# Performance work log

Hardware: AMD Instinct MI355X
Metric: run time of the kernel (lower is better)

The kernel has to match this reference:

```python
import jax, jax.numpy as jnp
import numpy as np

B, V, N, IN_F, HEADS, OUT_F = 4, 4, 1000, 64, 4, 32
D = HEADS * OUT_F  # 128, concat=True
E = 64000
NEG_SLOPE = 0.2


def setup_inputs() -> dict:
    key = jax.random.key(0)
    ks = jax.random.split(key, 8)
    x = jax.random.normal(ks[0], (B, V, N, IN_F), jnp.float32)
    edge_index = jax.random.randint(ks[1], (2, E), 0, B * N, dtype=jnp.int64)
    W = jax.random.normal(ks[2], (HEADS * OUT_F, IN_F), jnp.float32) / np.sqrt(IN_F)
    att = jax.random.normal(ks[3], (1, HEADS, 2 * OUT_F), jnp.float32) * 0.1
    in_proj_w = jax.random.normal(ks[4], (3 * D, D), jnp.float32) / np.sqrt(D)
    in_proj_b = jnp.zeros((3 * D,), jnp.float32)
    out_proj_w = jax.random.normal(ks[5], (D, D), jnp.float32) / np.sqrt(D)
    out_proj_b = jnp.zeros((D,), jnp.float32)
    bias = jnp.zeros((D,), jnp.float32)
    return dict(x=x, W=W, att=att, in_proj_w=in_proj_w, in_proj_b=in_proj_b,
                out_proj_w=out_proj_w, out_proj_b=out_proj_b, bias=bias,
                edge_index=edge_index)


def reference(x, W, att, in_proj_w, in_proj_b, out_proj_w, out_proj_b, bias, edge_index):
    Bx, Vx, Nx, _ = x.shape
    Ntot = Bx * Nx
    # intra-view GAT: shared W across views
    h = jnp.einsum('bvni,oi->bvno', x, W).reshape(Bx, Vx, Nx, HEADS, OUT_F)
    # block-diagonal placement: h_full[b*V+v, b*N:(b+1)*N] = h[b,v]
    ib = jnp.arange(Bx)
    hf = jnp.zeros((Bx, Vx, Bx, Nx, HEADS, OUT_F), x.dtype).at[ib, :, ib].set(h)
    h_full = hf.reshape(Bx * Vx, Ntot, HEADS, OUT_F)
    # add self loops
    loops = jnp.arange(Ntot, dtype=edge_index.dtype)
    src = jnp.concatenate([edge_index[0], loops])
    dst = jnp.concatenate([edge_index[1], loops])
    # attention scores (faithful to source: flatten h_full over (B*V, Ntot) and
    # index with raw node ids, i.e. gathers from block 0 only)
    h_flat = h_full.reshape(Bx * Vx * Ntot, HEADS, OUT_F)
    h_cat = jnp.concatenate([h_flat[src], h_flat[dst]], axis=-1)  # [Etot, H, 2*OUT]
    att_in = jax.nn.leaky_relu(h_cat, NEG_SLOPE)
    scores = jnp.sum(att * att_in, axis=-1)  # [Etot, HEADS]
    # per-destination segment softmax
    seg_max = jax.ops.segment_max(scores, dst, num_segments=Ntot)
    seg_max = jax.lax.stop_gradient(jnp.where(jnp.isfinite(seg_max), seg_max, 0.0))
    ex = jnp.exp(scores - seg_max[dst])
    denom = jax.ops.segment_sum(ex, dst, num_segments=Ntot)
    alpha = ex / (denom[dst] + 1e-16)  # [Etot, HEADS]
    # scatter-add aggregation, broadcast over B*V rows
    msgs = h_full[:, src] * alpha[None, :, :, None]  # [B*V, Etot, H, OUT]
    out_full = jnp.zeros_like(h_full).at[:, dst].add(msgs)
    # extract each graph's own node block
    out = out_full.reshape(Bx, Vx, Bx, Nx, HEADS, OUT_F)[ib, :, ib]  # [B,V,N,H,OUT]
    h_gat = out.reshape(Bx, Vx, Nx, HEADS * OUT_F)  # concat heads
    # inter-view mixing: MHA over the V axis per node
    seq = h_gat.transpose(0, 2, 1, 3).reshape(Bx * Nx, Vx, D)
    q, k, v = jnp.split(seq @ in_proj_w.T + in_proj_b, 3, axis=-1)
    hd = D // HEADS
    sp = lambda t: t.reshape(Bx * Nx, Vx, HEADS, hd).transpose(0, 2, 1, 3)
    q, k, v = sp(q), sp(k), sp(v)
    aw = jax.nn.softmax(jnp.einsum('bhqd,bhkd->bhqk', q, k) / jnp.sqrt(jnp.asarray(hd, x.dtype)), axis=-1)
    ao = jnp.einsum('bhqk,bhkd->bhqd', aw, v).transpose(0, 2, 1, 3).reshape(Bx * Nx, Vx, D)
    mixed = ao @ out_proj_w.T + out_proj_b
    h_mixed = mixed.reshape(Bx, Nx, Vx, D).transpose(0, 2, 1, 3)  # [B,V,N,D]
    return h_mixed + bias
```

## Files before the change

### kernel.cpp

```cpp
#include <hip/hip_runtime.h>

#define NN 1000
#define HEADS_ 4
#define DM 128
#define EE 64000
#define NTOT 4000
#define ETOT 68000
#define CAP 48
#define EB 34

template <int KK, int SCORE>
__device__ void gemm64(int mi, int ni,
                       const float* __restrict__ A, const float* __restrict__ Wt,
                       const float* __restrict__ b1,
                       float* __restrict__ C, int N,
                       const float* __restrict__ att,
                       float* __restrict__ ssrc, float* __restrict__ sdst) {
  __shared__ float As[64 * 64];
  __shared__ float Bs[64 * 64];
  int tid = threadIdx.x;
  int m0 = mi * 64, n0 = ni * 64;
  int tx = tid & 15, ty = tid >> 4;
  const float4* A4 = (const float4*)A;
  const float4* W4 = (const float4*)Wt;
  float acc[4][4] = {};

  for (int c = 0; c < KK / 64; ++c) {
    __syncthreads();
    {
      int q = tid & 15, r0 = tid >> 4;
#pragma unroll
      for (int p = 0; p < 4; ++p) {
        int r = r0 + p * 16;
        float4 v = A4[(size_t)(m0 + r) * (KK / 4) + c * 16 + q];
        *(float4*)&As[r * 64 + ((q ^ ((r >> 2) & 15)) << 2)] = v;
      }
#pragma unroll
      for (int p = 0; p < 4; ++p) {
        int r = r0 + p * 16;
        float4 v = W4[(size_t)(n0 + r) * (KK / 4) + c * 16 + q];
        *(float4*)&Bs[r * 64 + ((q ^ ((r >> 2) & 15)) << 2)] = v;
      }
    }
    __syncthreads();
#pragma unroll 4
    for (int q = 0; q < 16; ++q) {
      float4 a[4], b[4];
      int sa = (q ^ ty) << 2;
      int sb = (q ^ tx) << 2;
#pragma unroll
      for (int i = 0; i < 4; ++i)
        a[i] = *(const float4*)&As[(ty * 4 + i) * 64 + sa];
#pragma unroll
      for (int j = 0; j < 4; ++j)
        b[j] = *(const float4*)&Bs[(tx * 4 + j) * 64 + sb];
#pragma unroll
      for (int i = 0; i < 4; ++i)
#pragma unroll
        for (int j = 0; j < 4; ++j)
          acc[i][j] += a[i].x * b[j].x + a[i].y * b[j].y
                     + a[i].z * b[j].z + a[i].w * b[j].w;
    }
  }

  int nc = n0 + tx * 4;
  float4 bd = make_float4(0.f, 0.f, 0.f, 0.f);
  if (b1) bd = *(const float4*)&b1[nc];
#pragma unroll
  for (int i = 0; i < 4; ++i) {
    int m = m0 + ty * 4 + i;
    *(float4*)&C[(size_t)m * N + nc] =
        make_float4(acc[i][0] + bd.x, acc[i][1] + bd.y,
                    acc[i][2] + bd.z, acc[i][3] + bd.w);
  }

  if (SCORE && m0 < NN) {
    int hsel = tx >> 3;
    int h = ni * 2 + hsel;
    int kb = (tx & 7) * 4;
    float a0[4], a1[4];
#pragma unroll
    for (int j = 0; j < 4; ++j) {
      a0[j] = att[h * 64 + kb + j];
      a1[j] = att[h * 64 + 32 + kb + j];
    }
#pragma unroll
    for (int i = 0; i < 4; ++i) {
      int m = m0 + ty * 4 + i;
      float p0 = 0.f, p1 = 0.f;
#pragma unroll
      for (int j = 0; j < 4; ++j) {
        float g = acc[i][j];
        float lr = g > 0.f ? g : 0.2f * g;
        p0 += a0[j] * lr;
        p1 += a1[j] * lr;
      }
      p0 += __shfl_xor(p0, 1, 16); p1 += __shfl_xor(p1, 1, 16);
      p0 += __shfl_xor(p0, 2, 16); p1 += __shfl_xor(p1, 2, 16);
      p0 += __shfl_xor(p0, 4, 16); p1 += __shfl_xor(p1, 4, 16);
      if ((tx & 7) == 0 && m < NN) {
        ssrc[m * HEADS_ + h] = p0;
        sdst[m * HEADS_ + h] = p1;
      }
    }
  }
}

__global__ __launch_bounds__(256) void k1_kernel(const float* __restrict__ x,
                                                 const float* __restrict__ W,
                                                 const float* __restrict__ att,
                                                 float* __restrict__ hbuf,
                                                 float* __restrict__ ssrc,
                                                 float* __restrict__ sdst,
                                                 const int* __restrict__ ei,
                                                 int* __restrict__ cnt,
                                                 int* __restrict__ elist) {
  int bid = blockIdx.x;
  if (bid < 500) {
    gemm64<64, 1>(bid >> 1, bid & 1, x, W, nullptr, hbuf, 128, att, ssrc, sdst);
  } else {
    for (int e = (bid - 500) * 256 + threadIdx.x; e < ETOT; e += EB * 256) {
      int s, d;
      if (e < EE) { s = ei[e]; d = ei[EE + e]; }
      else { s = d = e - EE; }
      int pos = atomicAdd(&cnt[d], 1);
      if (pos < CAP) elist[d * CAP + pos] = s;
    }
  }
}

__global__ __launch_bounds__(256) void gather_kernel(const int* __restrict__ cnt,
                                                     const int* __restrict__ elist,
                                                     const float* __restrict__ ssrc,
                                                     const float* __restrict__ sdst,
                                                     const float* __restrict__ hbuf,
                                                     float* __restrict__ hgat) {
  __shared__ int   srcs[2][CAP];
  __shared__ float exs[2][CAP][HEADS_];
  int li = threadIdx.x >> 7;
  int t = threadIdx.x & 127;
  int d = blockIdx.x * 2 + li;
  int b = d / NN;
  int v = t >> 5, q = t & 31, h = q >> 3;
  int m = cnt[d]; if (m > CAP) m = CAP;
  for (int base = 0; base < m; base += 32) {
    int i = base + (t >> 2);
    if (i < m) {
      int s = elist[d * CAP + i];
      if ((t & 3) == 0) srcs[li][i] = s;
      float sc = ssrc[s * HEADS_ + (t & 3)] + sdst[d * HEADS_ + (t & 3)];
      exs[li][i][t & 3] = __expf(sc);
    }
  }
  __syncthreads();
  float den = 1e-16f;
  float4 acc = make_float4(0.f, 0.f, 0.f, 0.f);
  const float* hbase = hbuf + ((size_t)(b * 4 + v) * NN) * DM + q * 4;
  int i = 0;
  for (; i + 4 <= m; i += 4) {
    float ex[4]; unsigned sl[4]; float4 hv[4];
#pragma unroll
    for (int u = 0; u < 4; ++u) {
      ex[u] = exs[li][i + u][h];
      sl[u] = (unsigned)(srcs[li][i + u] - b * NN);
      unsigned sls = sl[u] < NN ? sl[u] : 0u;
      hv[u] = *(const float4*)(hbase + (size_t)sls * DM);
    }
#pragma unroll
    for (int u = 0; u < 4; ++u) {
      den += ex[u];
      float w = sl[u] < NN ? ex[u] : 0.f;
      acc.x += w * hv[u].x; acc.y += w * hv[u].y;
      acc.z += w * hv[u].z; acc.w += w * hv[u].w;
    }
  }
  for (; i < m; ++i) {
    float ex = exs[li][i][h];
    den += ex;
    unsigned sl = (unsigned)(srcs[li][i] - b * NN);
    if (sl < NN) {
      float4 hv = *(const float4*)(hbase + (size_t)sl * DM);
      acc.x += ex * hv.x; acc.y += ex * hv.y;
      acc.z += ex * hv.z; acc.w += ex * hv.w;
    }
  }
  float r = 1.f / den;
  acc.x *= r; acc.y *= r; acc.z *= r; acc.w *= r;
  *(float4*)&hgat[((size_t)(d * 4 + v)) * DM + q * 4] = acc;
}

__global__ __launch_bounds__(256) void qkv_kernel(const float* __restrict__ hgat,
                                                  const float* __restrict__ inw,
                                                  const float* __restrict__ inb,
                                                  float* __restrict__ qkv) {
  gemm64<128, 0>(blockIdx.x, blockIdx.y, hgat, inw, inb, qkv, 384,
                 nullptr, nullptr, nullptr);
}

__global__ __launch_bounds__(256) void attnout_kernel(const float* __restrict__ qkv,
                                                      const float* __restrict__ outw,
                                                      const float* __restrict__ outb,
                                                      const float* __restrict__ bias,
                                                      float* __restrict__ out) {
  __shared__ float smem[20480];
  float* outwS = smem;
  float* aoS   = smem + 16384;

  int tid = threadIdx.x;
  int blk = blockIdx.x;
  int cg = tid & 31, rg = tid >> 5;
  int node0 = blk * 8;

  const float4* Q4 = (const float4*)qkv;
  float4 qf[4], kf[4], vf[4];
#pragma unroll
  for (int vq = 0; vq < 4; ++vq) {
    size_t row = (size_t)((node0 + rg) * 4 + vq) * 96;
    qf[vq] = Q4[row + cg];
    kf[vq] = Q4[row + 32 + cg];
    vf[vq] = Q4[row + 64 + cg];
  }

  const float4* O4 = (const float4*)outw;
#pragma unroll
  for (int tt = 0; tt < 16; ++tt) {
    int g = tt * 256 + tid;
    int kg = g & 7, kc = (g >> 3) & 3, col = g >> 5;
    float4 vv = O4[g];
    *(float4*)&outwS[kc * 4096 + col * 32 + ((kg ^ ((col >> 2) & 7)) << 2)] = vv;
  }

  float S[4][4];
#pragma unroll
  for (int vq = 0; vq < 4; ++vq)
#pragma unroll
    for (int vk = 0; vk < 4; ++vk)
      S[vq][vk] = qf[vq].x * kf[vk].x + qf[vq].y * kf[vk].y
                + qf[vq].z * kf[vk].z + qf[vq].w * kf[vk].w;
#pragma unroll
  for (int vq = 0; vq < 4; ++vq)
#pragma unroll
    for (int vk = 0; vk < 4; ++vk) {
      float s = S[vq][vk];
      s += __shfl_xor(s, 1);
      s += __shfl_xor(s, 2);
      s += __shfl_xor(s, 4);
      S[vq][vk] = s * 0.17677669529663687f;
    }
#pragma unroll
  for (int vq = 0; vq < 4; ++vq) {
    float mx = fmaxf(fmaxf(S[vq][0], S[vq][1]), fmaxf(S[vq][2], S[vq][3]));
    float e0 = __expf(S[vq][0] - mx), e1 = __expf(S[vq][1] - mx);
    float e2 = __expf(S[vq][2] - mx), e3 = __expf(S[vq][3] - mx);
    float inv = 1.f / (e0 + e1 + e2 + e3);
    S[vq][0] = e0 * inv; S[vq][1] = e1 * inv; S[vq][2] = e2 * inv; S[vq][3] = e3 * inv;
  }

  {
    int kc = cg >> 3, d4 = cg & 7;
#pragma unroll
    for (int vq = 0; vq < 4; ++vq) {
      float4 o = make_float4(0.f, 0.f, 0.f, 0.f);
#pragma unroll
      for (int vk = 0; vk < 4; ++vk) {
        float w = S[vq][vk];
        o.x += w * vf[vk].x; o.y += w * vf[vk].y;
        o.z += w * vf[vk].z; o.w += w * vf[vk].w;
      }
      int r = rg * 4 + vq;
      *(float4*)&aoS[kc * 1024 + r * 32 + ((d4 ^ rg) << 2)] = o;
    }
  }
  __syncthreads();

  int rg2 = tid & 7, og = tid >> 3;
  float oc[4][4] = {};
#pragma unroll 2
  for (int kc2 = 0; kc2 < 4; ++kc2) {
#pragma unroll
    for (int q = 0; q < 8; ++q) {
      float4 a[4], bq[4];
      int ga = (q ^ rg2) << 2;
      int gb = (q ^ (og & 7)) << 2;
#pragma unroll
      for (int i = 0; i < 4; ++i)
        a[i] = *(const float4*)&aoS[kc2 * 1024 + (rg2 * 4 + i) * 32 + ga];
#pragma unroll
      for (int j = 0; j < 4; ++j)
        bq[j] = *(const float4*)&outwS[kc2 * 4096 + (og * 4 + j) * 32 + gb];
#pragma unroll
      for (int i = 0; i < 4; ++i)
#pragma unroll
        for (int j = 0; j < 4; ++j)
          oc[i][j] += a[i].x * bq[j].x + a[i].y * bq[j].y
                    + a[i].z * bq[j].z + a[i].w * bq[j].w;
    }
  }

  {
    int nc = og * 4;
    float4 ob = make_float4(outb[nc] + bias[nc], outb[nc + 1] + bias[nc + 1],
                            outb[nc + 2] + bias[nc + 2], outb[nc + 3] + bias[nc + 3]);
#pragma unroll
    for (int i = 0; i < 4; ++i) {
      int node = node0 + rg2, vv = i;
      int bg = node / NN, n = node - bg * NN;
      int om = (bg * 4 + vv) * NN + n;
      *(float4*)&out[(size_t)om * DM + nc] =
          make_float4(oc[i][0] + ob.x, oc[i][1] + ob.y,
                      oc[i][2] + ob.z, oc[i][3] + ob.w);
    }
  }
}

extern "C" void kernel_launch(void* const* d_in, const int* in_sizes, int n_in,
                              void* d_out, int out_size, void* d_ws, size_t ws_size,
                              hipStream_t stream) {
  const float* x    = (const float*)d_in[0];
  const float* W    = (const float*)d_in[1];
  const float* att  = (const float*)d_in[2];
  const float* inw  = (const float*)d_in[3];
  const float* inb  = (const float*)d_in[4];
  const float* outw = (const float*)d_in[5];
  const float* outb = (const float*)d_in[6];
  const float* bias = (const float*)d_in[7];
  const int*   ei   = (const int*)d_in[8];
  float* out = (float*)d_out;

  float* ws = (float*)d_ws;
  float* hbuf  = ws;
  float* hgat  = ws + 2100000;
  float* qkv   = ws + 4200000;
  float* ssrc  = ws + 12500000;
  float* sdst  = ssrc + 16000;
  int*   cnt   = (int*)(sdst + 16000);
  int*   elist = cnt + 4000;

  hipMemsetAsync(ssrc, 0, 36000 * sizeof(float), stream);

  k1_kernel<<<500 + EB, 256, 0, stream>>>(x, W, att, hbuf, ssrc, sdst, ei, cnt, elist);
  gather_kernel<<<NTOT / 2, 256, 0, stream>>>(cnt, elist, ssrc, sdst, hbuf, hgat);
  qkv_kernel<<<dim3(250, 6), 256, 0, stream>>>(hgat, inw, inb, qkv);
  attnout_kernel<<<500, 256, 0, stream>>>(qkv, outw, outb, bias, out);
}
```

Baseline: 148.5 us.

## Fuse GAT gather, QKV projection and view attention into one kernel

Merges the gather/softmax aggregation, the QKV GEMM and the inter-view attention plus output projection into a single kernel per pair of destination nodes. Intermediates stay in shared memory instead of making round trips through global hgat/qkv buffers, and two kernel launches are removed. In exchange, each 8-row block must stream the full in_proj and out_proj weights from cache in chunks, giving small, weight-bound GEMMs with many barriers.

```diff
diff --git a/kernel.cpp b/kernel.cpp
--- a/kernel.cpp
+++ b/kernel.cpp
@@ -12,7 +12,6 @@
 template <int KK, int SCORE>
 __device__ void gemm64(int mi, int ni,
                        const float* __restrict__ A, const float* __restrict__ Wt,
-                       const float* __restrict__ b1,
                        float* __restrict__ C, int N,
                        const float* __restrict__ att,
                        float* __restrict__ ssrc, float* __restrict__ sdst) {
@@ -64,14 +63,11 @@
   }
 
   int nc = n0 + tx * 4;
-  float4 bd = make_float4(0.f, 0.f, 0.f, 0.f);
-  if (b1) bd = *(const float4*)&b1[nc];
 #pragma unroll
   for (int i = 0; i < 4; ++i) {
     int m = m0 + ty * 4 + i;
     *(float4*)&C[(size_t)m * N + nc] =
-        make_float4(acc[i][0] + bd.x, acc[i][1] + bd.y,
-                    acc[i][2] + bd.z, acc[i][3] + bd.w);
+        make_float4(acc[i][0], acc[i][1], acc[i][2], acc[i][3]);
   }
 
   if (SCORE && m0 < NN) {
@@ -117,7 +113,7 @@
                                                  int* __restrict__ elist) {
   int bid = blockIdx.x;
   if (bid < 500) {
-    gemm64<64, 1>(bid >> 1, bid & 1, x, W, nullptr, hbuf, 128, att, ssrc, sdst);
+    gemm64<64, 1>(bid >> 1, bid & 1, x, W, hbuf, 128, att, ssrc, sdst);
   } else {
     for (int e = (bid - 500) * 256 + threadIdx.x; e < ETOT; e += EB * 256) {
       int s, d;
@@ -129,187 +125,183 @@
   }
 }
 
-__global__ __launch_bounds__(256) void gather_kernel(const int* __restrict__ cnt,
+__global__ __launch_bounds__(256) void gfuse2_kernel(const int* __restrict__ cnt,
                                                      const int* __restrict__ elist,
                                                      const float* __restrict__ ssrc,
                                                      const float* __restrict__ sdst,
                                                      const float* __restrict__ hbuf,
-                                                     float* __restrict__ hgat) {
-  __shared__ int   srcs[2][CAP];
-  __shared__ float exs[2][CAP][HEADS_];
-  int li = threadIdx.x >> 7;
-  int t = threadIdx.x & 127;
+                                                     const float* __restrict__ inw,
+                                                     const float* __restrict__ inb,
+                                                     const float* __restrict__ outw,
+                                                     const float* __restrict__ outb,
+                                                     const float* __restrict__ bias,
+                                                     float* __restrict__ out) {
+  __shared__ float smem[12352];
+  int*   srcs  = (int*)smem;
+  float* exs   = smem + 96;
+  float* hgatS = smem + 480;
+  float* qkvS  = smem + 1536;
+  float* inwS  = smem + 4672;
+  float* outwS = smem + 4672;
+  float* aoS   = smem + 8768;
+
+  int tid = threadIdx.x;
+  int li = tid >> 7;
+  int t = tid & 127;
   int d = blockIdx.x * 2 + li;
   int b = d / NN;
   int v = t >> 5, q = t & 31, h = q >> 3;
   int m = cnt[d]; if (m > CAP) m = CAP;
+
   for (int base = 0; base < m; base += 32) {
     int i = base + (t >> 2);
     if (i < m) {
       int s = elist[d * CAP + i];
-      if ((t & 3) == 0) srcs[li][i] = s;
+      if ((t & 3) == 0) srcs[li * CAP + i] = s;
       float sc = ssrc[s * HEADS_ + (t & 3)] + sdst[d * HEADS_ + (t & 3)];
-      exs[li][i][t & 3] = __expf(sc);
+      exs[li * 192 + i * 4 + (t & 3)] = __expf(sc);
     }
   }
   __syncthreads();
-  float den = 1e-16f;
-  float4 acc = make_float4(0.f, 0.f, 0.f, 0.f);
-  const float* hbase = hbuf + ((size_t)(b * 4 + v) * NN) * DM + q * 4;
-  int i = 0;
-  for (; i + 4 <= m; i += 4) {
-    float ex[4]; unsigned sl[4]; float4 hv[4];
-#pragma unroll
-    for (int u = 0; u < 4; ++u) {
-      ex[u] = exs[li][i + u][h];
-      sl[u] = (unsigned)(srcs[li][i + u] - b * NN);
-      unsigned sls = sl[u] < NN ? sl[u] : 0u;
-      hv[u] = *(const float4*)(hbase + (size_t)sls * DM);
-    }
-#pragma unroll
-    for (int u = 0; u < 4; ++u) {
-      den += ex[u];
-      float w = sl[u] < NN ? ex[u] : 0.f;
-      acc.x += w * hv[u].x; acc.y += w * hv[u].y;
-      acc.z += w * hv[u].z; acc.w += w * hv[u].w;
-    }
-  }
-  for (; i < m; ++i) {
-    float ex = exs[li][i][h];
-    den += ex;
-    unsigned sl = (unsigned)(srcs[li][i] - b * NN);
-    if (sl < NN) {
-      float4 hv = *(const float4*)(hbase + (size_t)sl * DM);
-      acc.x += ex * hv.x; acc.y += ex * hv.y;
-      acc.z += ex * hv.z; acc.w += ex * hv.w;
-    }
-  }
-  float r = 1.f / den;
-  acc.x *= r; acc.y *= r; acc.z *= r; acc.w *= r;
-  *(float4*)&hgat[((size_t)(d * 4 + v)) * DM + q * 4] = acc;
-}
-
-__global__ __launch_bounds__(256) void qkv_kernel(const float* __restrict__ hgat,
-                                                  const float* __restrict__ inw,
-                                                  const float* __restrict__ inb,
-                                                  float* __restrict__ qkv) {
-  gemm64<128, 0>(blockIdx.x, blockIdx.y, hgat, inw, inb, qkv, 384,
-                 nullptr, nullptr, nullptr);
-}
-
-__global__ __launch_bounds__(256) void attnout_kernel(const float* __restrict__ qkv,
-                                                      const float* __restrict__ outw,
-                                                      const float* __restrict__ outb,
-                                                      const float* __restrict__ bias,
-                                                      float* __restrict__ out) {
-  __shared__ float smem[20480];
-  float* outwS = smem;
-  float* aoS   = smem + 16384;
-
-  int tid = threadIdx.x;
-  int blk = blockIdx.x;
-  int cg = tid & 31, rg = tid >> 5;
-  int node0 = blk * 8;
-
-  const float4* Q4 = (const float4*)qkv;
-  float4 qf[4], kf[4], vf[4];
-#pragma unroll
-  for (int vq = 0; vq < 4; ++vq) {
-    size_t row = (size_t)((node0 + rg) * 4 + vq) * 96;
-    qf[vq] = Q4[row + cg];
-    kf[vq] = Q4[row + 32 + cg];
-    vf[vq] = Q4[row + 64 + cg];
-  }
-
-  const float4* O4 = (const float4*)outw;
-#pragma unroll
-  for (int tt = 0; tt < 16; ++tt) {
-    int g = tt * 256 + tid;
-    int kg = g & 7, kc = (g >> 3) & 3, col = g >> 5;
-    float4 vv = O4[g];
-    *(float4*)&outwS[kc * 4096 + col * 32 + ((kg ^ ((col >> 2) & 7)) << 2)] = vv;
-  }
-
-  float S[4][4];
-#pragma unroll
-  for (int vq = 0; vq < 4; ++vq)
-#pragma unroll
-    for (int vk = 0; vk < 4; ++vk)
-      S[vq][vk] = qf[vq].x * kf[vk].x + qf[vq].y * kf[vk].y
-                + qf[vq].z * kf[vk].z + qf[vq].w * kf[vk].w;
-#pragma unroll
-  for (int vq = 0; vq < 4; ++vq)
+  {
+    float den = 1e-16f;
+    float4 acc = make_float4(0.f, 0.f, 0.f, 0.f);
+    const float* hbase = hbuf + ((size_t)(b * 4 + v) * NN) * DM + q * 4;
+    int i = 0;
+    for (; i + 4 <= m; i += 4) {
+      float ex[4]; unsigned sl[4]; float4 hv[4];
+#pragma unroll
+      for (int u = 0; u < 4; ++u) {
+        ex[u] = exs[li * 192 + (i + u) * 4 + h];
+        sl[u] = (unsigned)(srcs[li * CAP + i + u] - b * NN);
+        unsigned sls = sl[u] < NN ? sl[u] : 0u;
+        hv[u] = *(const float4*)(hbase + (size_t)sls * DM);
+      }
+#pragma unroll
+      for (int u = 0; u < 4; ++u) {
+        den += ex[u];
+        float w = sl[u] < NN ? ex[u] : 0.f;
+        acc.x += w * hv[u].x; acc.y += w * hv[u].y;
+        acc.z += w * hv[u].z; acc.w += w * hv[u].w;
+      }
+    }
+    for (; i < m; ++i) {
+      float ex = exs[li * 192 + i * 4 + h];
+      den += ex;
+      unsigned sl = (unsigned)(srcs[li * CAP + i] - b * NN);
+      if (sl < NN) {
+        float4 hv = *(const float4*)(hbase + (size_t)sl * DM);
+        acc.x += ex * hv.x; acc.y += ex * hv.y;
+        acc.z += ex * hv.z; acc.w += ex * hv.w;
+      }
+    }
+    float r = 1.f / den;
+    *(float4*)&hgatS[(li * 4 + v) * 132 + q * 4] =
+        make_float4(acc.x * r, acc.y * r, acc.z * r, acc.w * r);
+  }
+  __syncthreads();
+
+  {
+    int l = tid & 63, w = tid >> 6;
+    int r = l & 7, cb = l >> 3;
+    float acc[12] = {};
+    const float4* I4 = (const float4*)inw;
+    for (int kc = 0; kc < 8; ++kc) {
+      __syncthreads();
+#pragma unroll
+      for (int p = 0; p < 6; ++p) {
+        int g = p * 256 + tid;
+        int c = g >> 2, kk = g & 3;
+        float4 vv = I4[(size_t)c * 32 + kc * 4 + kk];
+        *(float4*)&inwS[c * 20 + kk * 4] = vv;
+      }
+      __syncthreads();
+#pragma unroll
+      for (int kk = 0; kk < 4; ++kk) {
+        float4 a4 = *(const float4*)&hgatS[r * 132 + kc * 16 + kk * 4];
+#pragma unroll
+        for (int j = 0; j < 12; ++j) {
+          float4 b4 = *(const float4*)&inwS[(w * 96 + cb + 8 * j) * 20 + kk * 4];
+          acc[j] += a4.x * b4.x + a4.y * b4.y + a4.z * b4.z + a4.w * b4.w;
+        }
+      }
+    }
+#pragma unroll
+    for (int j = 0; j < 12; ++j) {
+      int c = w * 96 + cb + 8 * j;
+      qkvS[r * 392 + c] = acc[j] + inb[c];
+    }
+  }
+  __syncthreads();
+
+  {
+    float4 aq = *(const float4*)&qkvS[(li * 4 + v) * 392 + q * 4];
+    float S[4];
 #pragma unroll
     for (int vk = 0; vk < 4; ++vk) {
-      float s = S[vq][vk];
+      float4 kf = *(const float4*)&qkvS[(li * 4 + vk) * 392 + 128 + q * 4];
+      S[vk] = aq.x * kf.x + aq.y * kf.y + aq.z * kf.z + aq.w * kf.w;
+    }
+#pragma unroll
+    for (int vk = 0; vk < 4; ++vk) {
+      float s = S[vk];
       s += __shfl_xor(s, 1);
       s += __shfl_xor(s, 2);
       s += __shfl_xor(s, 4);
-      S[vq][vk] = s * 0.17677669529663687f;
-    }
-#pragma unroll
-  for (int vq = 0; vq < 4; ++vq) {
-    float mx = fmaxf(fmaxf(S[vq][0], S[vq][1]), fmaxf(S[vq][2], S[vq][3]));
-    float e0 = __expf(S[vq][0] - mx), e1 = __expf(S[vq][1] - mx);
-    float e2 = __expf(S[vq][2] - mx), e3 = __expf(S[vq][3] - mx);
-    float inv = 1.f / (e0 + e1 + e2 + e3);
-    S[vq][0] = e0 * inv; S[vq][1] = e1 * inv; S[vq][2] = e2 * inv; S[vq][3] = e3 * inv;
-  }
+      S[vk] = s * 0.17677669529663687f;
+    }
+    {
+      float mx = fmaxf(fmaxf(S[0], S[1]), fmaxf(S[2], S[3]));
+      float e0 = __expf(S[0] - mx), e1 = __expf(S[1] - mx);
+      float e2 = __expf(S[2] - mx), e3 = __expf(S[3] - mx);
+      float inv = 1.f / (e0 + e1 + e2 + e3);
+      S[0] = e0 * inv; S[1] = e1 * inv; S[2] = e2 * inv; S[3] = e3 * inv;
+    }
+    float4 ao = make_float4(0.f, 0.f, 0.f, 0.f);
+#pragma unroll
+    for (int vk = 0; vk < 4; ++vk) {
+      float w = S[vk];
+      float4 vf = *(const float4*)&qkvS[(li * 4 + vk) * 392 + 256 + q * 4];
+      ao.x += w * vf.x; ao.y += w * vf.y; ao.z += w * vf.z; ao.w += w * vf.w;
+    }
+    *(float4*)&aoS[li * 512 + v * 128 + q * 4] = ao;
+  }
+  __syncthreads();
 
   {
-    int kc = cg >> 3, d4 = cg & 7;
-#pragma unroll
-    for (int vq = 0; vq < 4; ++vq) {
-      float4 o = make_float4(0.f, 0.f, 0.f, 0.f);
-#pragma unroll
-      for (int vk = 0; vk < 4; ++vk) {
-        float w = S[vq][vk];
-        o.x += w * vf[vk].x; o.y += w * vf[vk].y;
-        o.z += w * vf[vk].z; o.w += w * vf[vk].w;
-      }
-      int r = rg * 4 + vq;
-      *(float4*)&aoS[kc * 1024 + r * 32 + ((d4 ^ rg) << 2)] = o;
-    }
-  }
-  __syncthreads();
-
-  int rg2 = tid & 7, og = tid >> 3;
-  float oc[4][4] = {};
-#pragma unroll 2
-  for (int kc2 = 0; kc2 < 4; ++kc2) {
-#pragma unroll
-    for (int q = 0; q < 8; ++q) {
-      float4 a[4], bq[4];
-      int ga = (q ^ rg2) << 2;
-      int gb = (q ^ (og & 7)) << 2;
-#pragma unroll
-      for (int i = 0; i < 4; ++i)
-        a[i] = *(const float4*)&aoS[kc2 * 1024 + (rg2 * 4 + i) * 32 + ga];
-#pragma unroll
-      for (int j = 0; j < 4; ++j)
-        bq[j] = *(const float4*)&outwS[kc2 * 4096 + (og * 4 + j) * 32 + gb];
-#pragma unroll
-      for (int i = 0; i < 4; ++i)
-#pragma unroll
-        for (int j = 0; j < 4; ++j)
-          oc[i][j] += a[i].x * bq[j].x + a[i].y * bq[j].y
-                    + a[i].z * bq[j].z + a[i].w * bq[j].w;
-    }
-  }
-
-  {
-    int nc = og * 4;
+    int rr = tid >> 5, oc = tid & 31;
+    int li2 = rr >> 2, v2 = rr & 3;
+    float occ4[4] = {};
+    const float4* O4 = (const float4*)outw;
+    for (int kc = 0; kc < 4; ++kc) {
+      if (kc) __syncthreads();
+#pragma unroll
+      for (int p = 0; p < 4; ++p) {
+        int g = p * 256 + tid;
+        int col = g >> 3, kg = g & 7;
+        float4 w4 = O4[(size_t)col * 32 + kc * 8 + kg];
+        *(float4*)&outwS[col * 32 + ((kg ^ ((col >> 2) & 7)) << 2)] = w4;
+      }
+      __syncthreads();
+#pragma unroll
+      for (int kg = 0; kg < 8; ++kg) {
+        float4 af = *(const float4*)&aoS[li2 * 512 + v2 * 128 + kc * 32 + kg * 4];
+#pragma unroll
+        for (int j = 0; j < 4; ++j) {
+          int c = oc * 4 + j;
+          float4 w4 = *(const float4*)&outwS[c * 32 + ((kg ^ (oc & 7)) << 2)];
+          occ4[j] += af.x * w4.x + af.y * w4.y + af.z * w4.z + af.w * w4.w;
+        }
+      }
+    }
+    int d2 = blockIdx.x * 2 + li2;
+    int b2 = d2 / NN, n2 = d2 - b2 * NN;
+    int om = (b2 * 4 + v2) * NN + n2;
+    int nc = oc * 4;
     float4 ob = make_float4(outb[nc] + bias[nc], outb[nc + 1] + bias[nc + 1],
                             outb[nc + 2] + bias[nc + 2], outb[nc + 3] + bias[nc + 3]);
-#pragma unroll
-    for (int i = 0; i < 4; ++i) {
-      int node = node0 + rg2, vv = i;
-      int bg = node / NN, n = node - bg * NN;
-      int om = (bg * 4 + vv) * NN + n;
-      *(float4*)&out[(size_t)om * DM + nc] =
-          make_float4(oc[i][0] + ob.x, oc[i][1] + ob.y,
-                      oc[i][2] + ob.z, oc[i][3] + ob.w);
-    }
+    *(float4*)&out[(size_t)om * DM + nc] =
+        make_float4(occ4[0] + ob.x, occ4[1] + ob.y, occ4[2] + ob.z, occ4[3] + ob.w);
   }
 }
 
@@ -329,8 +321,6 @@
 
   float* ws = (float*)d_ws;
   float* hbuf  = ws;
-  float* hgat  = ws + 2100000;
-  float* qkv   = ws + 4200000;
   float* ssrc  = ws + 12500000;
   float* sdst  = ssrc + 16000;
   int*   cnt   = (int*)(sdst + 16000);
@@ -339,7 +329,6 @@
   hipMemsetAsync(ssrc, 0, 36000 * sizeof(float), stream);
 
   k1_kernel<<<500 + EB, 256, 0, stream>>>(x, W, att, hbuf, ssrc, sdst, ei, cnt, elist);
-  gather_kernel<<<NTOT / 2, 256, 0, stream>>>(cnt, elist, ssrc, sdst, hbuf, hgat);
-  qkv_kernel<<<dim3(250, 6), 256, 0, stream>>>(hgat, inw, inb, qkv);
-  attnout_kernel<<<500, 256, 0, stream>>>(qkv, outw, outb, bias, out);
+  gfuse2_kernel<<<NTOT / 2, 256, 0, stream>>>(cnt, elist, ssrc, sdst, hbuf,
+                                              inw, inb, outw, outb, bias, out);
 }
```

Result: slower. 172.7 us (+16.3%).
